# Optimization experiments

Hardware: AMD Instinct MI355X
Metric: run time of the kernel (lower is better)

The kernel has to match this reference:

```python
import jax, jax.numpy as jnp
import numpy as np

D = 1024
H = 16
DH = D // H  # 64
B, S = 4, 1024


def setup_inputs() -> dict:
    key = jax.random.key(0)
    ks = jax.random.split(key, 7)
    sequences = jax.random.normal(ks[0], (B, S, D), dtype=jnp.float32)
    scale = 1.0 / np.sqrt(DH)
    Wq = jax.random.normal(ks[1], (H, DH, DH), dtype=jnp.float32) * scale
    Wk = jax.random.normal(ks[2], (H, DH, DH), dtype=jnp.float32) * scale
    Wv = jax.random.normal(ks[3], (H, DH, DH), dtype=jnp.float32) * scale
    bq = jax.random.normal(ks[4], (H, DH), dtype=jnp.float32) * 0.01
    bk = jax.random.normal(ks[5], (H, DH), dtype=jnp.float32) * 0.01
    bv = jax.random.normal(ks[6], (H, DH), dtype=jnp.float32) * 0.01
    return {"sequences": sequences, "Wq": Wq, "Wk": Wk, "Wv": Wv,
            "bq": bq, "bk": bk, "bv": bv}


def reference(sequences, Wq, Wk, Wv, bq, bk, bv):
    b, s, d = sequences.shape
    x = sequences.reshape(b, s, H, DH)  # split channels into heads
    # per-head Linear: y = x @ W.T + b (torch convention)
    q = jnp.einsum('bshd,hed->bshe', x, Wq) + bq
    k = jnp.einsum('bshd,hed->bshe', x, Wk) + bk
    v = jnp.einsum('bshd,hed->bshe', x, Wv) + bv
    inv_sqrt_dh = jnp.asarray(1.0 / np.sqrt(DH), dtype=sequences.dtype)
    scores = jnp.einsum('bshe,bthe->bhst', q, k) * inv_sqrt_dh  # [B,H,S,S]
    attn = jax.nn.softmax(scores, axis=-1)
    out = jnp.einsum('bhst,bthe->bshe', attn, v)  # [B,S,H,DH]
    return out.reshape(b, s, d)  # hstack of heads == reshape here
```

## Files before the change

kernel.cpp:

```cpp
#include <hip/hip_runtime.h>

#define H 16
#define DH 64
#define BB 4
#define SS 1024
#define DD 1024

typedef __attribute__((ext_vector_type(8))) short bf16x8;
typedef __attribute__((ext_vector_type(4))) float f32x4;
typedef __attribute__((ext_vector_type(4))) unsigned int u32x4;
typedef _Float16 f16x4 __attribute__((ext_vector_type(4)));
typedef _Float16 f16x8 __attribute__((ext_vector_type(8)));
typedef __fp16 hf16x2 __attribute__((ext_vector_type(2)));

#define QSCALE 0.18033688011112042f

#if __has_builtin(__builtin_amdgcn_exp2f)
__device__ __forceinline__ float fast_exp2(float x) {
    return __builtin_amdgcn_exp2f(x);
}
#else
__device__ __forceinline__ float fast_exp2(float x) {
    float r;
    asm("v_exp_f32 %0, %1" : "=v"(r) : "v"(x));
    return r;
}
#endif

__device__ __forceinline__ unsigned short f2bf(float f) {
    union { float f; unsigned u; } v; v.f = f;
    unsigned u = v.u;
    return (unsigned short)((u + 0x7FFFu + ((u >> 16) & 1u)) >> 16);
}

__device__ __forceinline__ unsigned short f2h(float f) {
    union { _Float16 h; unsigned short u; } v;
    v.h = (_Float16)f;
    return v.u;
}

__device__ __forceinline__ void pack8(unsigned short* dst, f32x4 a, f32x4 b) {
    unsigned u0 = (unsigned)f2bf(a[0]) | ((unsigned)f2bf(a[1]) << 16);
    unsigned u1 = (unsigned)f2bf(a[2]) | ((unsigned)f2bf(a[3]) << 16);
    unsigned u2 = (unsigned)f2bf(b[0]) | ((unsigned)f2bf(b[1]) << 16);
    unsigned u3 = (unsigned)f2bf(b[2]) | ((unsigned)f2bf(b[3]) << 16);
    u32x4 v = {u0, u1, u2, u3};
    *(u32x4*)dst = v;
}

__device__ __forceinline__ void async_cp1k(const unsigned short* g,
                                           unsigned short* l, int lane) {
    __builtin_amdgcn_global_load_lds(
        (const __attribute__((address_space(1))) unsigned int*)(g + lane * 8),
        (__attribute__((address_space(3))) unsigned int*)l, 16, 0, 0);
}

__global__ __launch_bounds__(256) void wprep_kernel(
    const float* __restrict__ Wq, const float* __restrict__ Wk,
    const float* __restrict__ Wv, unsigned short* __restrict__ Wp)
{
    const int tg = blockIdx.x * 256 + threadIdx.x;
    const int r = tg >> 2, part = tg & 3;
    const int e = r & 63, hm = r >> 6;
    const int m = hm % 3, h = hm / 3;
    const float* src = (m == 0 ? Wq : (m == 1 ? Wk : Wv)) +
                       (size_t)(h * 64 + e) * 64 + part * 16;
    const float scale = (m == 0) ? QSCALE : 1.0f;
    f32x4 f0 = ((const f32x4*)src)[0];
    f32x4 f1 = ((const f32x4*)src)[1];
    f32x4 f2 = ((const f32x4*)src)[2];
    f32x4 f3 = ((const f32x4*)src)[3];
    f0 *= scale; f1 *= scale; f2 *= scale; f3 *= scale;
    unsigned short tmp[16];
    pack8(tmp, f0, f1);
    pack8(tmp + 8, f2, f3);
    unsigned short* dst = Wp + (size_t)(hm * 64 + e) * 64;
    const int c0 = part * 2, sw = e & 7;
    *(u32x4*)(dst + (c0 ^ sw) * 8)       = *(const u32x4*)tmp;
    *(u32x4*)(dst + ((c0 + 1) ^ sw) * 8) = *(const u32x4*)(tmp + 8);
}

__global__ __launch_bounds__(256) void qkv_kernel(
    const float* __restrict__ x, const unsigned short* __restrict__ Wp,
    const float* __restrict__ bq, const float* __restrict__ bk,
    const float* __restrict__ bv,
    unsigned short* __restrict__ Qg, unsigned short* __restrict__ Kg,
    unsigned short* __restrict__ VTg)
{
    __shared__ __align__(16) unsigned short Xl[4096];
    __shared__ __align__(16) unsigned short Wl[12288];

    const int bid = blockIdx.x;
    const int sc = bid & 15, h = (bid >> 4) & 15, b = bid >> 8;
    const int s0 = sc * 64;
    const int tid = threadIdx.x;
    const int lane = tid & 63, w = tid >> 6;

    {
        const unsigned short* wbase = Wp + (size_t)h * 12288;
#pragma unroll
        for (int sub = 0; sub < 6; sub++) {
            const int off = w * 3072 + sub * 512;
            async_cp1k(wbase + off, &Wl[off], lane);
        }
    }
    {
        const int s = tid >> 2, part = tid & 3;
        const float* src = x + ((size_t)(b * SS + s0 + s)) * DD + h * DH + part * 16;
        f32x4 f0 = ((const f32x4*)src)[0];
        f32x4 f1 = ((const f32x4*)src)[1];
        f32x4 f2 = ((const f32x4*)src)[2];
        f32x4 f3 = ((const f32x4*)src)[3];
        unsigned short tmp[16];
        pack8(tmp, f0, f1);
        pack8(tmp + 8, f2, f3);
        const int c0 = part * 2, sws = s & 7;
        *(u32x4*)&Xl[s * 64 + (c0 ^ sws) * 8]       = *(const u32x4*)tmp;
        *(u32x4*)&Xl[s * 64 + ((c0 + 1) ^ sws) * 8] = *(const u32x4*)(tmp + 8);
    }
    __syncthreads();

    const int l15 = lane & 15, quad = lane >> 4, sw = l15 & 7;

    f32x4 acc[3][4];
#pragma unroll
    for (int m = 0; m < 3; m++)
#pragma unroll
        for (int nt = 0; nt < 4; nt++) acc[m][nt] = (f32x4){0.f, 0.f, 0.f, 0.f};

#pragma unroll
    for (int k2 = 0; k2 < 2; k2++) {
        const int csw = (((k2 << 2) | quad) ^ sw) * 8;
        bf16x8 a = *(const bf16x8*)&Xl[(w * 16 + l15) * 64 + csw];
#pragma unroll
        for (int nt = 0; nt < 4; nt++) {
            const int boff = (nt * 16 + l15) * 64 + csw;
            bf16x8 b0 = *(const bf16x8*)&Wl[boff];
            acc[0][nt] = __builtin_amdgcn_mfma_f32_16x16x32_bf16(a, b0, acc[0][nt], 0, 0, 0);
            bf16x8 b1 = *(const bf16x8*)&Wl[4096 + boff];
            acc[1][nt] = __builtin_amdgcn_mfma_f32_16x16x32_bf16(a, b1, acc[1][nt], 0, 0, 0);
            bf16x8 b2 = *(const bf16x8*)&Wl[8192 + boff];
            acc[2][nt] = __builtin_amdgcn_mfma_f32_16x16x32_bf16(a, b2, acc[2][nt], 0, 0, 0);
        }
    }
    __syncthreads();

#pragma unroll
    for (int nt = 0; nt < 4; nt++) {
        const int e = nt * 16 + l15;
        const float bqs = bq[h * DH + e] * QSCALE;
        const float bks = bk[h * DH + e];
        const float bvs = bv[h * DH + e];
#pragma unroll
        for (int r = 0; r < 4; r++) {
            const int srow = w * 16 + quad * 4 + r;
            Xl[srow * 64 + e] = f2bf(acc[0][nt][r] + bqs);
            Wl[srow * 64 + e] = f2bf(acc[1][nt][r] + bks);
            Wl[4096 + e * 64 + quad * 16 + w * 4 + r] = f2h(acc[2][nt][r] + bvs);
        }
    }
    __syncthreads();
    {
        const size_t bh = (size_t)(b * H + h);
        const int row = tid >> 2, part = tid & 3;
        const int cg = part * 16, c0 = part * 2, swr = row & 7;
        unsigned short* qdst = Qg + (bh * SS + s0 + row) * DH + cg;
        *(u32x4*)qdst       = *(const u32x4*)&Xl[row * 64 + cg];
        *(u32x4*)(qdst + 8) = *(const u32x4*)&Xl[row * 64 + cg + 8];
        unsigned short* kbase = Kg + (bh * 16 + sc) * 4096 + row * 64;
        *(u32x4*)(kbase + (c0 ^ swr) * 8)       = *(const u32x4*)&Wl[row * 64 + c0 * 8];
        *(u32x4*)(kbase + ((c0 + 1) ^ swr) * 8) = *(const u32x4*)&Wl[row * 64 + c0 * 8 + 8];
        unsigned short* vbase = VTg + (bh * 16 + sc) * 4096 + row * 64;
        *(u32x4*)(vbase + (c0 ^ swr) * 8)       = *(const u32x4*)&Wl[4096 + row * 64 + c0 * 8];
        *(u32x4*)(vbase + ((c0 + 1) ^ swr) * 8) = *(const u32x4*)&Wl[4096 + row * 64 + c0 * 8 + 8];
    }
}

__global__ __launch_bounds__(256) void attn_kernel(
    const unsigned short* __restrict__ Qg, const unsigned short* __restrict__ Kg,
    const unsigned short* __restrict__ VTg, float* __restrict__ out)
{
    __shared__ __align__(16) unsigned short Kl0[4096], Kl1[4096];
    __shared__ __align__(16) unsigned short Vl0[4096], Vl1[4096];

    const int bid = blockIdx.x;
    const int bh = bid & 63, qt = bid >> 6;
    const int h = bh & 15, b = bh >> 4;
    const int tid = threadIdx.x;
    const int lane = tid & 63, w = tid >> 6;
    const int l15 = lane & 15, quad = lane >> 4, sw = l15 & 7;

    const unsigned short* Kt = Kg + (size_t)bh * 16 * 4096;
    const unsigned short* Vt = VTg + (size_t)bh * 16 * 4096;

    const int kb0 = l15 * 64 + ((quad)     ^ sw) * 8;
    const int kb1 = l15 * 64 + ((4 | quad) ^ sw) * 8;
    const int vb0 = l15 * 64 + (((quad << 1))     ^ sw) * 8;
    const int vb1 = l15 * 64 + (((quad << 1) | 1) ^ sw) * 8;

    bf16x8 aQ0, aQ1;
    {
        const int qrow = qt * 64 + w * 16 + l15;
        const unsigned short* qp = Qg + ((size_t)bh * SS + qrow) * DH + quad * 8;
        aQ0 = *(const bf16x8*)(qp);
        aQ1 = *(const bf16x8*)(qp + 32);
    }

    {
        const int off = w * 1024;
        async_cp1k(Kt + off,       Kl0 + off,       lane);
        async_cp1k(Kt + off + 512, Kl0 + off + 512, lane);
        async_cp1k(Vt + off,       Vl0 + off,       lane);
        async_cp1k(Vt + off + 512, Vl0 + off + 512, lane);
    }

    f32x4 accO[4];
#pragma unroll
    for (int et = 0; et < 4; et++) accO[et] = (f32x4){0.f, 0.f, 0.f, 0.f};
    float rs_acc = 0.f;

    auto step = [&](int kt, const unsigned short* Kc, const unsigned short* Vc,
                    unsigned short* Kn, unsigned short* Vn) {
        __syncthreads();
        if (kt < 15) {
            const unsigned short* kg = Kt + (kt + 1) * 4096;
            const unsigned short* vg = Vt + (kt + 1) * 4096;
            const int off = w * 1024;
            async_cp1k(kg + off,       Kn + off,       lane);
            async_cp1k(kg + off + 512, Kn + off + 512, lane);
            async_cp1k(vg + off,       Vn + off,       lane);
            async_cp1k(vg + off + 512, Vn + off + 512, lane);
        }

        bf16x8 aK[4][2];
#pragma unroll
        for (int nt = 0; nt < 4; nt++) {
            aK[nt][0] = *(const bf16x8*)(Kc + kb0 + nt * 1024);
            aK[nt][1] = *(const bf16x8*)(Kc + kb1 + nt * 1024);
        }
        f16x8 aV01[4], aV23[4];
#pragma unroll
        for (int et = 0; et < 4; et++) {
            aV01[et] = *(const f16x8*)(Vc + vb0 + et * 1024);
            aV23[et] = *(const f16x8*)(Vc + vb1 + et * 1024);
        }

        f32x4 sc[4];
#pragma unroll
        for (int nt = 0; nt < 4; nt++) {
            f32x4 z = {0.f, 0.f, 0.f, 0.f};
            z = __builtin_amdgcn_mfma_f32_16x16x32_bf16(aK[nt][0], aQ0, z, 0, 0, 0);
            z = __builtin_amdgcn_mfma_f32_16x16x32_bf16(aK[nt][1], aQ1, z, 0, 0, 0);
            sc[nt] = z;
        }

        float rs = 0.f;
        f16x4 pf[4];
#pragma unroll
        for (int nt = 0; nt < 4; nt++) {
            float p0 = fast_exp2(sc[nt][0]);
            float p1 = fast_exp2(sc[nt][1]);
            float p2 = fast_exp2(sc[nt][2]);
            float p3 = fast_exp2(sc[nt][3]);
            rs += (p0 + p1) + (p2 + p3);
            union { hf16x2 h; unsigned u; } lo, hi;
            lo.h = __builtin_amdgcn_cvt_pkrtz(p0, p1);
            hi.h = __builtin_amdgcn_cvt_pkrtz(p2, p3);
            union { unsigned u[2]; f16x4 v; } pk;
            pk.u[0] = lo.u; pk.u[1] = hi.u;
            pf[nt] = pk.v;
        }
        rs_acc += rs;

#pragma unroll
        for (int et = 0; et < 4; et++) {
            f16x4 v0 = __builtin_shufflevector(aV01[et], aV01[et], 0, 1, 2, 3);
            f16x4 v1 = __builtin_shufflevector(aV01[et], aV01[et], 4, 5, 6, 7);
            f16x4 v2 = __builtin_shufflevector(aV23[et], aV23[et], 0, 1, 2, 3);
            f16x4 v3 = __builtin_shufflevector(aV23[et], aV23[et], 4, 5, 6, 7);
            accO[et] = __builtin_amdgcn_mfma_f32_16x16x16f16(v0, pf[0], accO[et], 0, 0, 0);
            accO[et] = __builtin_amdgcn_mfma_f32_16x16x16f16(v1, pf[1], accO[et], 0, 0, 0);
            accO[et] = __builtin_amdgcn_mfma_f32_16x16x16f16(v2, pf[2], accO[et], 0, 0, 0);
            accO[et] = __builtin_amdgcn_mfma_f32_16x16x16f16(v3, pf[3], accO[et], 0, 0, 0);
        }
    };

    for (int i = 0; i < 8; i++) {
        step(2 * i,     Kl0, Vl0, Kl1, Vl1);
        step(2 * i + 1, Kl1, Vl1, Kl0, Vl0);
    }

    {
        float rs = rs_acc;
        rs += __shfl_xor(rs, 16);
        rs += __shfl_xor(rs, 32);
        const float inv = 1.0f / rs;
        const int srow = qt * 64 + w * 16 + l15;
        float* op = out + ((size_t)b * SS + srow) * DD + h * DH;
#pragma unroll
        for (int et = 0; et < 4; et++) {
            f32x4 v = accO[et] * inv;
            *(f32x4*)(op + et * 16 + quad * 4) = v;
        }
    }
}

extern "C" void kernel_launch(void* const* d_in, const int* in_sizes, int n_in,
                              void* d_out, int out_size, void* d_ws, size_t ws_size,
                              hipStream_t stream) {
    const float* x  = (const float*)d_in[0];
    const float* Wq = (const float*)d_in[1];
    const float* Wk = (const float*)d_in[2];
    const float* Wv = (const float*)d_in[3];
    const float* bq = (const float*)d_in[4];
    const float* bk = (const float*)d_in[5];
    const float* bv = (const float*)d_in[6];

    const size_t NE = (size_t)BB * H * SS * DH;
    unsigned short* Qg  = (unsigned short*)d_ws;
    unsigned short* Kg  = Qg + NE;
    unsigned short* VTg = Kg + NE;
    unsigned short* Wp  = VTg + NE;

    wprep_kernel<<<48, 256, 0, stream>>>(Wq, Wk, Wv, Wp);
    qkv_kernel<<<BB * H * (SS / 64), 256, 0, stream>>>(x, Wp, bq, bk, bv,
                                                       Qg, Kg, VTg);
    attn_kernel<<<BB * H * 16, 256, 0, stream>>>(Qg, Kg, VTg, (float*)d_out);
}
```

Before: 117.4 us.

## Triple-buffer K/V tiles with partial vmcnt waits and single barrier

Replaces the double-buffered K/V LDS ring with a three-slot ring and fully unrolls the 16-step loop. Before each step it issues the async copy for the next tile, waits only until at most four loads remain outstanding, then barriers. This lets the prefetch overlap the current tile's compute instead of forcing all copies to drain at __syncthreads. It raises LDS use by 16 KB per block, which may lower occupancy, and relies on hand-encoded waitcnt values being correct for this target.

New measurement: 130.3 us. 11.0% more time.

```diff
diff --git a/kernel.cpp b/kernel.cpp
--- a/kernel.cpp
+++ b/kernel.cpp
@@ -14,6 +14,9 @@
 typedef __fp16 hf16x2 __attribute__((ext_vector_type(2)));
 
 #define QSCALE 0.18033688011112042f
+
+#define WAITCNT_VM4 0x0F74
+#define WAITCNT_VM0 0x0F70
 
 #if __has_builtin(__builtin_amdgcn_exp2f)
 __device__ __forceinline__ float fast_exp2(float x) {
@@ -180,8 +183,8 @@
     const unsigned short* __restrict__ Qg, const unsigned short* __restrict__ Kg,
     const unsigned short* __restrict__ VTg, float* __restrict__ out)
 {
-    __shared__ __align__(16) unsigned short Kl0[4096], Kl1[4096];
-    __shared__ __align__(16) unsigned short Vl0[4096], Vl1[4096];
+    __shared__ __align__(16) unsigned short Kl[3][4096];
+    __shared__ __align__(16) unsigned short Vl[3][4096];
 
     const int bid = blockIdx.x;
     const int bh = bid & 63, qt = bid >> 6;
@@ -208,10 +211,10 @@
 
     {
         const int off = w * 1024;
-        async_cp1k(Kt + off,       Kl0 + off,       lane);
-        async_cp1k(Kt + off + 512, Kl0 + off + 512, lane);
-        async_cp1k(Vt + off,       Vl0 + off,       lane);
-        async_cp1k(Vt + off + 512, Vl0 + off + 512, lane);
+        async_cp1k(Kt + off,       Kl[0] + off,       lane);
+        async_cp1k(Kt + off + 512, Kl[0] + off + 512, lane);
+        async_cp1k(Vt + off,       Vl[0] + off,       lane);
+        async_cp1k(Vt + off + 512, Vl[0] + off + 512, lane);
     }
 
     f32x4 accO[4];
@@ -219,18 +222,24 @@
     for (int et = 0; et < 4; et++) accO[et] = (f32x4){0.f, 0.f, 0.f, 0.f};
     float rs_acc = 0.f;
 
-    auto step = [&](int kt, const unsigned short* Kc, const unsigned short* Vc,
-                    unsigned short* Kn, unsigned short* Vn) {
-        __syncthreads();
+#pragma unroll
+    for (int kt = 0; kt < 16; kt++) {
         if (kt < 15) {
+            const int nb = (kt + 1) % 3;
             const unsigned short* kg = Kt + (kt + 1) * 4096;
             const unsigned short* vg = Vt + (kt + 1) * 4096;
             const int off = w * 1024;
-            async_cp1k(kg + off,       Kn + off,       lane);
-            async_cp1k(kg + off + 512, Kn + off + 512, lane);
-            async_cp1k(vg + off,       Vn + off,       lane);
-            async_cp1k(vg + off + 512, Vn + off + 512, lane);
-        }
+            async_cp1k(kg + off,       Kl[nb] + off,       lane);
+            async_cp1k(kg + off + 512, Kl[nb] + off + 512, lane);
+            async_cp1k(vg + off,       Vl[nb] + off,       lane);
+            async_cp1k(vg + off + 512, Vl[nb] + off + 512, lane);
+        }
+        if (kt == 15) __builtin_amdgcn_s_waitcnt(WAITCNT_VM0);
+        else          __builtin_amdgcn_s_waitcnt(WAITCNT_VM4);
+        __builtin_amdgcn_s_barrier();
+
+        const unsigned short* Kc = Kl[kt % 3];
+        const unsigned short* Vc = Vl[kt % 3];
 
         bf16x8 aK[4][2];
 #pragma unroll
@@ -283,11 +292,6 @@
             accO[et] = __builtin_amdgcn_mfma_f32_16x16x16f16(v2, pf[2], accO[et], 0, 0, 0);
             accO[et] = __builtin_amdgcn_mfma_f32_16x16x16f16(v3, pf[3], accO[et], 0, 0, 0);
         }
-    };
-
-    for (int i = 0; i < 8; i++) {
-        step(2 * i,     Kl0, Vl0, Kl1, Vl1);
-        step(2 * i + 1, Kl1, Vl1, Kl0, Vl0);
     }
 
     {
```
